# Optimization experiments

Measured on AMD Instinct MI355X. Metric: run time of the kernel, lower is better.

## Reference

```python
import jax, jax.numpy as jnp
import numpy as np

B, R, C, D = 8, 64, 16, 128  # batch, num_rows(taxa), patch_num, embed_dim


def _linear_init(key, fan_in, fan_out):
    lim = 1.0 / np.sqrt(fan_in)
    kw, kb = jax.random.split(key)
    W = jax.random.uniform(kw, (fan_in, fan_out), jnp.float32, -lim, lim)
    b = jax.random.uniform(kb, (fan_out,), jnp.float32, -lim, lim)
    return W, b


def setup_inputs() -> dict:
    key = jax.random.key(0)
    ks = jax.random.split(key, 8)
    row_np, col_np = np.triu_indices(R, k=1)  # n = R*(R-1)/2 = 2016 pairs
    hW, hb = _linear_init(ks[1], D, D)
    gW, gb = _linear_init(ks[2], D, D)
    qW, qb = _linear_init(ks[3], D, D)
    kW, kb = _linear_init(ks[4], D, D)
    s1W, s1b = _linear_init(ks[5], D, D)
    s2W, s2b = _linear_init(ks[6], D, 1)
    return {
        "batch_input": jax.random.normal(ks[0], (B, R, C, D), jnp.float32),
        "seq_mask": jnp.ones((B, 1, C), jnp.float32),
        "row": jnp.asarray(row_np, jnp.int32),
        "col": jnp.asarray(col_np, jnp.int32),
        "hW": hW, "hb": hb, "gW": gW, "gb": gb,
        "qW": qW, "qb": qb, "kW": kW, "kb": kb,
        "s1W": s1W, "s1b": s1b, "s2W": s2W, "s2b": s2b,
    }


def reference(batch_input, seq_mask, row, col,
              hW, hb, gW, gb, qW, qb, kW, kb, s1W, s1b, s2W, s2b):
    b, r, c, d = batch_input.shape
    n = row.shape[0]
    # pairwise gather: x_i, x_j -> [b, n, c, d]
    x_i = batch_input[:, row]
    x_j = batch_input[:, col]
    # sigmoid gate fusion of the pair
    h = (x_i - x_j) @ hW + hb
    z = jax.nn.sigmoid(h)
    x = z * x_i + (1.0 - z) * x_j
    # masked global attention over the batch_input 'memory' (r > 2 branch)
    q = x @ qW + qb                    # [b, n, c, d]
    k = batch_input @ kW + kb          # [b, r, c, d]
    scale = 1.0 / np.sqrt(d * c).astype(np.float32)
    alpha = jnp.einsum('bncd,brcd->bnr', q, k) * scale
    # -inf at (pair n, rows row[n] and col[n]); equivalent to += -inf on finite scores
    neg_mask = (jnp.zeros((n, r), bool)
                .at[jnp.arange(n), row].set(True)
                .at[jnp.arange(n), col].set(True))
    alpha = jnp.where(neg_mask[None], -jnp.inf, alpha)
    alpha = jax.nn.softmax(alpha, axis=-1)
    x_glob = jnp.einsum('bnr,brcd->bncd', alpha, batch_input)
    g = x_glob @ gW + gb
    w = jax.nn.sigmoid(g)
    x = (1.0 - w) * x + w * x_glob
    # s_out: Linear -> GELU(exact) -> Linear(d,1), then mask and reduce over c
    s = jax.nn.gelu(x @ s1W + s1b, approximate=False) @ s2W + s2b  # [b, n, c, 1]
    scores = s[..., 0] * seq_mask       # seq_mask [b,1,c] broadcasts over n
    return scores.sum(-1)               # [b, n]
```

## Files before the change

kernel.cpp:

```cpp
#include <hip/hip_runtime.h>
#include <hip/hip_bf16.h>
#include <math.h>

#define B_    8
#define R_    64
#define C_    16
#define D_    128
#define NPAIR 2016
#define CD    2048
#define PG    16
#define NPG   126
#define XSTR  136
#define LSTR  68
#define NEG_BIG (-1e30f)
#define SCALE 0.022097086912079608f

typedef __attribute__((ext_vector_type(8))) short short8;
typedef __attribute__((ext_vector_type(4))) float float4v;

#define WMH  0u
#define WML  16384u
#define WHH  32768u
#define WHL  49152u
#define WGH  65536u
#define WGL  81920u
#define WSH  98304u
#define VECO 131072u
#define QBKO 131592u
#define MO   132616u
#define XTO  1181192u
#define GTO  2229768u
#define HO   3278344u

__device__ __forceinline__ unsigned short f2b(float f){
    union { float f; unsigned int u; } v; v.f = f;
    const unsigned int r = v.u + 0x7FFFu + ((v.u >> 16) & 1u);
    return (unsigned short)(r >> 16);
}
__device__ __forceinline__ float b2f(unsigned short u){
    union { unsigned int i; float f; } v; v.i = ((unsigned int)u) << 16; return v.f;
}
__device__ __forceinline__ float lo2f(unsigned int u){
    union { unsigned int i; float f; } v; v.i = u << 16; return v.f;
}
__device__ __forceinline__ float hif2f(unsigned int u){
    union { unsigned int i; float f; } v; v.i = u & 0xffff0000u; return v.f;
}
__device__ __forceinline__ unsigned int pack2(float a, float b){
    unsigned int r;
    asm("v_cvt_pk_bf16_f32 %0, %1, %2" : "=v"(r) : "v"(a), "v"(b));
    return r;
}
__device__ __forceinline__ unsigned short f2b1(float a){
    unsigned int r;
    asm("v_cvt_pk_bf16_f32 %0, %1, %1" : "=v"(r) : "v"(a));
    return (unsigned short)r;
}
__device__ __forceinline__ void split_bf(float v, float* hi, float* lo){
    union { float f; unsigned int u; } x; x.f = v;
    const unsigned int r = (x.u + 0x7FFFu + ((x.u >> 16) & 1u)) & 0xffff0000u;
    union { unsigned int u; float f; } h; h.u = r;
    *hi = h.f; *lo = v - h.f;
}
__device__ __forceinline__ float sigmoid_safe(float x){
    return __builtin_amdgcn_rcpf(1.f + __expf(-x));
}
__device__ __forceinline__ float gelu_tanh(float x){
    const float u = x*x;
    const float g2 = x*(1.5957691216057308f + 0.07135481627159f*u);
    return x * sigmoid_safe(g2);
}

__global__ __launch_bounds__(256) void k_prepA(
    const float* __restrict__ x,
    const float* __restrict__ hW, const float* __restrict__ gW,
    const float* __restrict__ qW, const float* __restrict__ qb,
    const float* __restrict__ kW, const float* __restrict__ kb,
    unsigned short* __restrict__ ws)
{
    __shared__ __align__(16) unsigned short tile[128*69];
    const int bid = blockIdx.x, t = threadIdx.x;
    if (bid < 64){
        __shared__ float sKW[2][128];
        const int e0 = bid*2;
        sKW[t>>7][t&127] = kW[(e0 + (t>>7))*128 + (t&127)];
        __syncthreads();
        const int e = t>>7, d = t&127;
        const float* qr = qW + d*128;
        const float* kr = sKW[e];
        float acc = 0.f;
        #pragma unroll 8
        for (int g = 0; g < 128; g += 4){
            const float4 qv = *reinterpret_cast<const float4*>(qr + g);
            acc += qv.x*kr[g] + qv.y*kr[g+1] + qv.z*kr[g+2] + qv.w*kr[g+3];
        }
        float hi, lo; split_bf(acc, &hi, &lo);
        ws[WMH + d*128 + (e0+e)] = f2b(hi);
        ws[WML + d*128 + (e0+e)] = f2b(lo);
    } else if (bid == 64){
        float* vec = (float*)(ws + VECO);
        if (t < 128){
            float a1 = 0.f, a2 = 0.f;
            #pragma unroll 8
            for (int g = 0; g < 128; g += 4){
                const float4 q4 = *reinterpret_cast<const float4*>(qW + t*128 + g);
                const float4 k4 = *reinterpret_cast<const float4*>(kW + t*128 + g);
                const float4 kb4 = *reinterpret_cast<const float4*>(kb + g);
                const float4 qb4 = *reinterpret_cast<const float4*>(qb + g);
                a1 += q4.x*kb4.x + q4.y*kb4.y + q4.z*kb4.z + q4.w*kb4.w;
                a2 += k4.x*qb4.x + k4.y*qb4.y + k4.z*qb4.z + k4.w*qb4.w;
            }
            vec[t] = a1;
            vec[128 + t] = a2;
        } else if (t == 128){
            float a = 0.f;
            for (int g = 0; g < 128; ++g) a = fmaf(qb[g], kb[g], a);
            vec[256] = a;
        }
    } else if (bid < 193){
        const int j = bid - 65;
        const int mat = j >> 6;
        const int gid = (j & 63)*256 + t;
        const int n = gid >> 7, k = gid & 127;
        const float* W = (mat==0) ? hW : gW;
        const unsigned int baseh = (mat==0) ? WHH : WGH;
        const unsigned int basel = (mat==0) ? WHL : WGL;
        float hi, lo; split_bf(W[k*128 + n], &hi, &lo);
        ws[baseh + gid] = f2b(hi);
        ws[basel + gid] = f2b(lo);
    } else {
        const int blk = bid - 193;
        const int b = blk >> 4, cd0 = (blk & 15)*128;
        #pragma unroll
        for (int i = 0; i < 32; ++i){
            const int idx = i*256 + t;
            const int r = idx >> 7, cc = idx & 127;
            tile[cc*69 + r] = f2b(x[((size_t)(b*64 + r))*CD + cd0 + cc]);
        }
        __syncthreads();
        const unsigned int base = XTO + (unsigned int)(b*2048 + cd0)*64;
        #pragma unroll
        for (int j = 0; j < 32; ++j){
            const int idx = j*256 + t;
            const int cc = idx >> 6, r = idx & 63;
            ws[base + cc*64 + r] = tile[cc*69 + r];
        }
    }
}

__global__ __launch_bounds__(512) void k_prepB(const float* __restrict__ x,
        const float* __restrict__ gb, const float* __restrict__ s1W,
        unsigned short* __restrict__ ws)
{
    __shared__ __align__(16) unsigned short smem[8832];
    __shared__ float sQ[4];
    const int bid = blockIdx.x, t = threadIdx.x;
    const int w = t >> 6, lane = t & 63, l15 = lane & 15, quad = lane >> 4;

    if (bid < 256){
        const bool isM = (bid >= 128);
        unsigned short* sH = smem;
        const int br0 = (bid & 127) * 4;
        const float* kqf = (const float*)(ws + VECO) + 128;
        const float* mbf = (const float*)(ws + VECO);
        if (t < 4) sQ[t] = 0.f;
        __syncthreads();
        float qacc[4] = {0.f, 0.f, 0.f, 0.f};
        #pragma unroll
        for (int i = 0; i < 4; ++i){
            const int flat = (t + 512*i)*4;
            const int lr = i;
            const int cd = flat & 2047;
            const float4 v = *reinterpret_cast<const float4*>(x + (size_t)(br0+lr)*CD + cd);
            const int ad = (lr*16 + (cd>>7))*XSTR + lr*8 + (cd & 127);
            uint2 uh;
            uh.x = pack2(v.x, v.y); uh.y = pack2(v.z, v.w);
            *reinterpret_cast<uint2*>(sH + ad) = uh;
            if (isM){
                const float4 kq4 = *reinterpret_cast<const float4*>(kqf + (cd & 127));
                qacc[i] = v.x*kq4.x + v.y*kq4.y + v.z*kq4.z + v.w*kq4.w;
            }
        }
        if (isM){
            #pragma unroll
            for (int i = 0; i < 4; ++i){
                float s = qacc[i];
                #pragma unroll
                for (int off = 1; off < 64; off <<= 1) s += __shfl_xor(s, off);
                if (lane == 0) atomicAdd(&sQ[i], s);
            }
        }
        __syncthreads();
        const unsigned short* Bh = isM ? (ws+WMH) : (ws+WHH);
        const unsigned short* Bl = isM ? (ws+WML) : (ws+WHL);
        const float bv = isM ? mbf[w*16 + l15] : 0.f;
        float4v acc[4];
        #pragma unroll
        for (int mt = 0; mt < 4; ++mt){ float4v d = {bv,bv,bv,bv}; acc[mt] = d; }
        #pragma unroll
        for (int ks = 0; ks < 4; ++ks){
            const int ko = ks*32 + quad*8;
            const int bd = (w*16 + l15)*128 + ko;
            const short8 bh = *reinterpret_cast<const short8*>(Bh + bd);
            const short8 bl = *reinterpret_cast<const short8*>(Bl + bd);
            #pragma unroll
            for (int mt = 0; mt < 4; ++mt){
                const int ad = (mt*16 + l15)*XSTR + mt*8 + ko;
                const short8 ah = *reinterpret_cast<const short8*>(sH + ad);
                float4v d = acc[mt];
                d = __builtin_amdgcn_mfma_f32_16x16x32_bf16(ah, bh, d, 0,0,0);
                d = __builtin_amdgcn_mfma_f32_16x16x32_bf16(ah, bl, d, 0,0,0);
                acc[mt] = d;
            }
        }
        const int f = w*16 + l15;
        const unsigned int dsto = isM ? MO : HO;
        #pragma unroll
        for (int mt = 0; mt < 4; ++mt)
        #pragma unroll
        for (int e = 0; e < 4; ++e){
            const int c = quad*4 + e;
            ws[dsto + (size_t)(br0+mt)*CD + c*128 + f] = f2b(acc[mt][e]);
        }
        if (isM && t < 4){
            const float s0 = ((const float*)(ws + VECO))[256];
            ((float*)(ws + QBKO))[br0 + t] = sQ[t] + 16.f*s0;
        }
    } else if (bid < 384){
        unsigned short* tileB = smem;
        const int gidx = bid - 256;
        const int b = gidx >> 4, cd0 = (gidx & 15)*128;
        #pragma unroll
        for (int i = 0; i < 16; ++i){
            const int idx = i*512 + t;
            const int r = idx >> 7, dd = idx & 127;
            tileB[r*138 + dd] = f2b(x[(size_t)(b*64 + r)*CD + cd0 + dd]);
        }
        __syncthreads();
        float4v acc[4];
        #pragma unroll
        for (int nt = 0; nt < 4; ++nt){ float4v z = {0.f,0.f,0.f,0.f}; acc[nt] = z; }
        #pragma unroll
        for (int ks = 0; ks < 4; ++ks){
            const int ko = ks*32 + quad*8;
            const int adg = (w*16 + l15)*128 + ko;
            const short8 ah = *reinterpret_cast<const short8*>(ws + WGH + adg);
            const short8 al = *reinterpret_cast<const short8*>(ws + WGL + adg);
            #pragma unroll
            for (int nt = 0; nt < 4; ++nt){
                const short8 bb = *reinterpret_cast<const short8*>(tileB + (nt*16 + l15)*138 + ko);
                float4v d = acc[nt];
                d = __builtin_amdgcn_mfma_f32_16x16x32_bf16(ah, bb, d, 0,0,0);
                d = __builtin_amdgcn_mfma_f32_16x16x32_bf16(al, bb, d, 0,0,0);
                acc[nt] = d;
            }
        }
        #pragma unroll
        for (int nt = 0; nt < 4; ++nt)
        #pragma unroll
        for (int e = 0; e < 4; ++e){
            const int f = w*16 + quad*4 + e;
            const float val = acc[nt][e] + gb[f];
            ws[GTO + (size_t)(b*2048 + cd0 + f)*64 + nt*16 + l15] = f2b(val);
        }
    } else {
        const int gid = (bid - 384)*4096 + t;
        #pragma unroll
        for (int i = 0; i < 8; ++i){
            const int g = gid + i*512;
            const int n = g >> 7, k = g & 127;
            ws[WSH + g] = f2b(s1W[k*128 + n]);
        }
    }
}

__global__ __launch_bounds__(512, 4) void k_main(
    const float* __restrict__ x, const float* __restrict__ seq_mask,
    const int* __restrict__ row, const int* __restrict__ col,
    const float* __restrict__ hb, const float* __restrict__ s1b,
    const float* __restrict__ s2W, const float* __restrict__ s2b,
    const unsigned short* __restrict__ ws, float* __restrict__ out)
{
    __shared__ __align__(16) unsigned short sX[256*XSTR + 128];
    __shared__ __align__(16) unsigned short sAl[16*72];
    __shared__ float sLog[16*LSTR];
    __shared__ float sOut[PG];
    __shared__ float sMask[16];
    __shared__ int srp[PG], scp[PG];

    const int t = threadIdx.x;
    const int w = t >> 6, lane = t & 63, l15 = lane & 15, quad = lane >> 4;
    const int b = blockIdx.x, p0 = blockIdx.y * PG;
    const float* xb = x + (size_t)b * R_ * CD;
    const unsigned short* Hb = ws + HO + (size_t)b * R_ * CD;

    if (t < PG){ srp[t] = row[p0+t]; scp[t] = col[p0+t]; sOut[t] = 0.f; }
    if (t >= 32 && t < 48) sMask[t-32] = seq_mask[b*C_ + (t-32)];
    for (int i = t; i < 1152; i += 512) sAl[i] = 0;
    for (int i = t; i < 16*LSTR; i += 512) sLog[i] = 0.f;
    __syncthreads();

    #pragma unroll 4
    for (int i = 0; i < 16; ++i){
        const int flat = (t + 512*i)*4;
        const int p = flat >> 11, cd = flat & 2047;
        const int ri = srp[p], ci = scp[p];
        const float4 xi = *reinterpret_cast<const float4*>(xb + (size_t)ri*CD + cd);
        const float4 xj = *reinterpret_cast<const float4*>(xb + (size_t)ci*CD + cd);
        const uint2 Hi2 = *reinterpret_cast<const uint2*>(Hb + (size_t)ri*CD + cd);
        const uint2 Hj2 = *reinterpret_cast<const uint2*>(Hb + (size_t)ci*CD + cd);
        const float4 h4 = *reinterpret_cast<const float4*>(hb + (cd & 127));
        const float z0 = sigmoid_safe(lo2f(Hi2.x)  - lo2f(Hj2.x)  + h4.x);
        const float z1 = sigmoid_safe(hif2f(Hi2.x) - hif2f(Hj2.x) + h4.y);
        const float z2 = sigmoid_safe(lo2f(Hi2.y)  - lo2f(Hj2.y)  + h4.z);
        const float z3 = sigmoid_safe(hif2f(Hi2.y) - hif2f(Hj2.y) + h4.w);
        const float v0 = xj.x + z0*(xi.x - xj.x);
        const float v1 = xj.y + z1*(xi.y - xj.y);
        const float v2 = xj.z + z2*(xi.z - xj.z);
        const float v3 = xj.w + z3*(xi.w - xj.w);
        const int ad = (p*16 + (cd>>7))*XSTR + p*8 + (cd & 127);
        uint2 uv; uv.x = pack2(v0,v1); uv.y = pack2(v2,v3);
        *reinterpret_cast<uint2*>(sX + ad) = uv;
    }
    __syncthreads();

    {
        const int rt = w & 3, kh = w >> 2;
        const int r = rt*16 + l15;
        const unsigned short* Mr = ws + MO + ((size_t)b*64 + r)*CD + kh*1024;
        float4v d0 = {0.f,0.f,0.f,0.f}, d1 = {0.f,0.f,0.f,0.f};
        float4v d2 = {0.f,0.f,0.f,0.f}, d3 = {0.f,0.f,0.f,0.f};
        #pragma unroll
        for (int ks = 0; ks < 32; ks += 4){
            #pragma unroll
            for (int u = 0; u < 4; ++u){
                const int k = kh*1024 + (ks+u)*32 + quad*8;
                const short8 ah = *reinterpret_cast<const short8*>(
                    sX + (l15*16 + (k>>7))*XSTR + l15*8 + (k & 127));
                const short8 bh = *reinterpret_cast<const short8*>(Mr + (ks+u)*32 + quad*8);
                if (u == 0) d0 = __builtin_amdgcn_mfma_f32_16x16x32_bf16(ah, bh, d0, 0,0,0);
                else if (u == 1) d1 = __builtin_amdgcn_mfma_f32_16x16x32_bf16(ah, bh, d1, 0,0,0);
                else if (u == 2) d2 = __builtin_amdgcn_mfma_f32_16x16x32_bf16(ah, bh, d2, 0,0,0);
                else d3 = __builtin_amdgcn_mfma_f32_16x16x32_bf16(ah, bh, d3, 0,0,0);
            }
        }
        const float4v d = (d0 + d1) + (d2 + d3);
        #pragma unroll
        for (int e = 0; e < 4; ++e){
            const int pp = quad*4 + e;
            atomicAdd(&sLog[pp*LSTR + r], d[e]);
        }
    }
    __syncthreads();

    const unsigned short* XTb = ws + XTO + (size_t)b * CD * 64;
    const unsigned short* GTb = ws + GTO + (size_t)b * CD * 64;
    short8 px0[2], px1[2], pg0[2], pg1[2];
    #pragma unroll
    for (int j = 0; j < 2; ++j){
        const int cd = w*256 + j*16 + l15;
        px0[j] = *reinterpret_cast<const short8*>(XTb + (size_t)cd*64 + quad*8);
        px1[j] = *reinterpret_cast<const short8*>(XTb + (size_t)cd*64 + 32 + quad*8);
        pg0[j] = *reinterpret_cast<const short8*>(GTb + (size_t)cd*64 + quad*8);
        pg1[j] = *reinterpret_cast<const short8*>(GTb + (size_t)cd*64 + 32 + quad*8);
    }

    if (t < 256){
        const int pp = t >> 4, l = t & 15;
        const int ri = srp[pp], ci = scp[pp];
        const float* qbk = (const float*)(ws + QBKO);
        float v[4]; float m = NEG_BIG;
        #pragma unroll
        for (int k = 0; k < 4; ++k){
            const int r = l + 16*k;
            float lv = (sLog[pp*LSTR + r] + qbk[b*64 + r]) * SCALE;
            if (r == ri || r == ci) lv = NEG_BIG;
            v[k] = lv; m = fmaxf(m, lv);
        }
        #pragma unroll
        for (int s = 1; s < 16; s <<= 1) m = fmaxf(m, __shfl_xor(m, s));
        float e4[4]; float sum = 0.f;
        #pragma unroll
        for (int k = 0; k < 4; ++k){
            const int r = l + 16*k;
            const bool masked = (r == ri || r == ci);
            const float e = masked ? 0.f : __expf(fmaxf(v[k]-m, -80.f));
            e4[k] = e; sum += e;
        }
        #pragma unroll
        for (int s = 1; s < 16; s <<= 1) sum += __shfl_xor(sum, s);
        const float inv = __builtin_amdgcn_rcpf(sum);
        #pragma unroll
        for (int k = 0; k < 4; ++k) sAl[pp*72 + l + 16*k] = f2b1(e4[k]*inv);
    }
    __syncthreads();

    {
        const short8 Ah0 = *reinterpret_cast<const short8*>(sAl + l15*72 + quad*8);
        const short8 Ah1 = *reinterpret_cast<const short8*>(sAl + l15*72 + 32 + quad*8);
        #pragma unroll
        for (int j = 0; j < 16; ++j){
            const int s = j & 1;
            float4v dx = {0.f,0.f,0.f,0.f}, dg = {0.f,0.f,0.f,0.f};
            dx = __builtin_amdgcn_mfma_f32_16x16x32_bf16(Ah0, px0[s], dx, 0,0,0);
            dx = __builtin_amdgcn_mfma_f32_16x16x32_bf16(Ah1, px1[s], dx, 0,0,0);
            dg = __builtin_amdgcn_mfma_f32_16x16x32_bf16(Ah0, pg0[s], dg, 0,0,0);
            dg = __builtin_amdgcn_mfma_f32_16x16x32_bf16(Ah1, pg1[s], dg, 0,0,0);
            if (j + 2 < 16){
                const int cd2 = w*256 + (j+2)*16 + l15;
                px0[s] = *reinterpret_cast<const short8*>(XTb + (size_t)cd2*64 + quad*8);
                px1[s] = *reinterpret_cast<const short8*>(XTb + (size_t)cd2*64 + 32 + quad*8);
                pg0[s] = *reinterpret_cast<const short8*>(GTb + (size_t)cd2*64 + quad*8);
                pg1[s] = *reinterpret_cast<const short8*>(GTb + (size_t)cd2*64 + 32 + quad*8);
            }
            const int cd = w*256 + j*16 + l15;
            #pragma unroll
            for (int e = 0; e < 4; ++e){
                const int pp = quad*4 + e;
                const int ad = (pp*16 + (cd>>7))*XSTR + pp*8 + (cd & 127);
                const float wv = sigmoid_safe(dg[e]);
                const float xo = b2f(sX[ad]);
                sX[ad] = f2b1((1.f - wv)*xo + wv*dx[e]);
            }
        }
    }
    __syncthreads();

    {
        float4v acc16[16];
        const float bv = s1b[w*16 + l15];
        #pragma unroll
        for (int mt = 0; mt < 16; ++mt){ float4v d = {bv,bv,bv,bv}; acc16[mt] = d; }
        #pragma unroll
        for (int ks = 0; ks < 4; ++ks){
            const int ko = ks*32 + quad*8;
            const int bd = (w*16 + l15)*128 + ko;
            const short8 bh = *reinterpret_cast<const short8*>(ws + WSH + bd);
            #pragma unroll
            for (int mt = 0; mt < 16; ++mt){
                const short8 a = *reinterpret_cast<const short8*>(sX + (mt*16 + l15)*XSTR + mt*8 + ko);
                acc16[mt] = __builtin_amdgcn_mfma_f32_16x16x32_bf16(a, bh, acc16[mt], 0,0,0);
            }
        }
        const float s2v = s2W[w*16 + l15];
        const float mk0 = sMask[quad*4+0], mk1 = sMask[quad*4+1];
        const float mk2 = sMask[quad*4+2], mk3 = sMask[quad*4+3];
        float psum[16];
        #pragma unroll
        for (int mt = 0; mt < 16; ++mt){
            float s = gelu_tanh(acc16[mt][0]) * mk0;
            s += gelu_tanh(acc16[mt][1]) * mk1;
            s += gelu_tanh(acc16[mt][2]) * mk2;
            s += gelu_tanh(acc16[mt][3]) * mk3;
            psum[mt] = s * s2v;
        }
        #pragma unroll
        for (int s = 1; s < 64; s <<= 1)
            #pragma unroll
            for (int mt = 0; mt < 16; ++mt) psum[mt] += __shfl_xor(psum[mt], s);
        if (lane == 0){
            #pragma unroll
            for (int mt = 0; mt < 16; ++mt) atomicAdd(&sOut[mt], psum[mt]);
        }
    }
    __syncthreads();

    if (t < PG){
        float msum = 0.f;
        #pragma unroll
        for (int c = 0; c < 16; ++c) msum += sMask[c];
        out[(size_t)b*NPAIR + p0 + t] = sOut[t] + s2b[0]*msum;
    }
}

extern "C" void kernel_launch(void* const* d_in, const int* in_sizes, int n_in,
                              void* d_out, int out_size, void* d_ws, size_t ws_size,
                              hipStream_t stream)
{
    const float* x    = (const float*)d_in[0];
    const float* mask = (const float*)d_in[1];
    const int*   row  = (const int*)d_in[2];
    const int*   col  = (const int*)d_in[3];
    const float* hW  = (const float*)d_in[4];  const float* hb  = (const float*)d_in[5];
    const float* gW  = (const float*)d_in[6];  const float* gb  = (const float*)d_in[7];
    const float* qW  = (const float*)d_in[8];  const float* qb  = (const float*)d_in[9];
    const float* kW  = (const float*)d_in[10]; const float* kb  = (const float*)d_in[11];
    const float* s1W = (const float*)d_in[12]; const float* s1b = (const float*)d_in[13];
    const float* s2W = (const float*)d_in[14]; const float* s2b = (const float*)d_in[15];

    unsigned short* ws = (unsigned short*)d_ws;

    k_prepA<<<321, 256, 0, stream>>>(x, hW, gW, qW, qb, kW, kb, ws);
    k_prepB<<<388, 512, 0, stream>>>(x, gb, s1W, ws);
    k_main<<<dim3(B_, NPG), 512, 0, stream>>>(x, mask, row, col,
                                              hb, s1b, s2W, s2b,
                                              ws, (float*)d_out);
}
```

Baseline: 226.1 us.

## Fold hW/gW bf16 splitting and x transpose into prepB; batch B-operand loads

```diff
diff --git a/kernel.cpp b/kernel.cpp
--- a/kernel.cpp
+++ b/kernel.cpp
@@ -20,10 +20,6 @@
 
 #define WMH  0u
 #define WML  16384u
-#define WHH  32768u
-#define WHL  49152u
-#define WGH  65536u
-#define WGL  81920u
 #define WSH  98304u
 #define VECO 131072u
 #define QBKO 131592u
@@ -62,6 +58,13 @@
     union { unsigned int u; float f; } h; h.u = r;
     *hi = h.f; *lo = v - h.f;
 }
+__device__ __forceinline__ void splitw(float v, short* h, short* l){
+    union { float f; unsigned int u; } x; x.f = v;
+    const unsigned int rh = (x.u + 0x7FFFu + ((x.u >> 16) & 1u)) & 0xffff0000u;
+    union { unsigned int u; float f; } hf; hf.u = rh;
+    *h = (short)(rh >> 16);
+    *l = (short)f2b(v - hf.f);
+}
 __device__ __forceinline__ float sigmoid_safe(float x){
     return __builtin_amdgcn_rcpf(1.f + __expf(-x));
 }
@@ -72,13 +75,10 @@
 }
 
 __global__ __launch_bounds__(256) void k_prepA(
-    const float* __restrict__ x,
-    const float* __restrict__ hW, const float* __restrict__ gW,
     const float* __restrict__ qW, const float* __restrict__ qb,
     const float* __restrict__ kW, const float* __restrict__ kb,
     unsigned short* __restrict__ ws)
 {
-    __shared__ __align__(16) unsigned short tile[128*69];
     const int bid = blockIdx.x, t = threadIdx.x;
     if (bid < 64){
         __shared__ float sKW[2][128];
@@ -97,7 +97,7 @@
         float hi, lo; split_bf(acc, &hi, &lo);
         ws[WMH + d*128 + (e0+e)] = f2b(hi);
         ws[WML + d*128 + (e0+e)] = f2b(lo);
-    } else if (bid == 64){
+    } else {
         float* vec = (float*)(ws + VECO);
         if (t < 128){
             float a1 = 0.f, a2 = 0.f;
@@ -117,38 +117,11 @@
             for (int g = 0; g < 128; ++g) a = fmaf(qb[g], kb[g], a);
             vec[256] = a;
         }
-    } else if (bid < 193){
-        const int j = bid - 65;
-        const int mat = j >> 6;
-        const int gid = (j & 63)*256 + t;
-        const int n = gid >> 7, k = gid & 127;
-        const float* W = (mat==0) ? hW : gW;
-        const unsigned int baseh = (mat==0) ? WHH : WGH;
-        const unsigned int basel = (mat==0) ? WHL : WGL;
-        float hi, lo; split_bf(W[k*128 + n], &hi, &lo);
-        ws[baseh + gid] = f2b(hi);
-        ws[basel + gid] = f2b(lo);
-    } else {
-        const int blk = bid - 193;
-        const int b = blk >> 4, cd0 = (blk & 15)*128;
-        #pragma unroll
-        for (int i = 0; i < 32; ++i){
-            const int idx = i*256 + t;
-            const int r = idx >> 7, cc = idx & 127;
-            tile[cc*69 + r] = f2b(x[((size_t)(b*64 + r))*CD + cd0 + cc]);
-        }
-        __syncthreads();
-        const unsigned int base = XTO + (unsigned int)(b*2048 + cd0)*64;
-        #pragma unroll
-        for (int j = 0; j < 32; ++j){
-            const int idx = j*256 + t;
-            const int cc = idx >> 6, r = idx & 63;
-            ws[base + cc*64 + r] = tile[cc*69 + r];
-        }
     }
 }
 
 __global__ __launch_bounds__(512) void k_prepB(const float* __restrict__ x,
+        const float* __restrict__ hW, const float* __restrict__ gW,
         const float* __restrict__ gb, const float* __restrict__ s1W,
         unsigned short* __restrict__ ws)
 {
@@ -191,40 +164,71 @@
             }
         }
         __syncthreads();
-        const unsigned short* Bh = isM ? (ws+WMH) : (ws+WHH);
-        const unsigned short* Bl = isM ? (ws+WML) : (ws+WHL);
-        const float bv = isM ? mbf[w*16 + l15] : 0.f;
-        float4v acc[4];
-        #pragma unroll
-        for (int mt = 0; mt < 4; ++mt){ float4v d = {bv,bv,bv,bv}; acc[mt] = d; }
-        #pragma unroll
-        for (int ks = 0; ks < 4; ++ks){
-            const int ko = ks*32 + quad*8;
-            const int bd = (w*16 + l15)*128 + ko;
-            const short8 bh = *reinterpret_cast<const short8*>(Bh + bd);
-            const short8 bl = *reinterpret_cast<const short8*>(Bl + bd);
-            #pragma unroll
-            for (int mt = 0; mt < 4; ++mt){
-                const int ad = (mt*16 + l15)*XSTR + mt*8 + ko;
-                const short8 ah = *reinterpret_cast<const short8*>(sH + ad);
-                float4v d = acc[mt];
-                d = __builtin_amdgcn_mfma_f32_16x16x32_bf16(ah, bh, d, 0,0,0);
-                d = __builtin_amdgcn_mfma_f32_16x16x32_bf16(ah, bl, d, 0,0,0);
-                acc[mt] = d;
-            }
-        }
-        const int f = w*16 + l15;
-        const unsigned int dsto = isM ? MO : HO;
-        #pragma unroll
-        for (int mt = 0; mt < 4; ++mt)
-        #pragma unroll
-        for (int e = 0; e < 4; ++e){
-            const int c = quad*4 + e;
-            ws[dsto + (size_t)(br0+mt)*CD + c*128 + f] = f2b(acc[mt][e]);
-        }
-        if (isM && t < 4){
-            const float s0 = ((const float*)(ws + VECO))[256];
-            ((float*)(ws + QBKO))[br0 + t] = sQ[t] + 16.f*s0;
+        if (isM){
+            const float bv = mbf[w*16 + l15];
+            float4v acc[4];
+            #pragma unroll
+            for (int mt = 0; mt < 4; ++mt){ float4v d = {bv,bv,bv,bv}; acc[mt] = d; }
+            #pragma unroll
+            for (int ks = 0; ks < 4; ++ks){
+                const int ko = ks*32 + quad*8;
+                const int bd = (w*16 + l15)*128 + ko;
+                const short8 bh = *reinterpret_cast<const short8*>(ws + WMH + bd);
+                const short8 bl = *reinterpret_cast<const short8*>(ws + WML + bd);
+                #pragma unroll
+                for (int mt = 0; mt < 4; ++mt){
+                    const int ad = (mt*16 + l15)*XSTR + mt*8 + ko;
+                    const short8 ah = *reinterpret_cast<const short8*>(sH + ad);
+                    float4v d = acc[mt];
+                    d = __builtin_amdgcn_mfma_f32_16x16x32_bf16(ah, bh, d, 0,0,0);
+                    d = __builtin_amdgcn_mfma_f32_16x16x32_bf16(ah, bl, d, 0,0,0);
+                    acc[mt] = d;
+                }
+            }
+            const int f = w*16 + l15;
+            #pragma unroll
+            for (int mt = 0; mt < 4; ++mt)
+            #pragma unroll
+            for (int e = 0; e < 4; ++e){
+                const int c = quad*4 + e;
+                ws[MO + (size_t)(br0+mt)*CD + c*128 + f] = f2b(acc[mt][e]);
+            }
+            if (t < 4){
+                const float s0 = ((const float*)(ws + VECO))[256];
+                ((float*)(ws + QBKO))[br0 + t] = sQ[t] + 16.f*s0;
+            }
+        } else {
+            const int n = w*16 + l15;
+            float4v acc[4];
+            #pragma unroll
+            for (int mt = 0; mt < 4; ++mt){ float4v z = {0.f,0.f,0.f,0.f}; acc[mt] = z; }
+            #pragma unroll
+            for (int ks = 0; ks < 4; ++ks){
+                const int ko = ks*32 + quad*8;
+                short8 bh, bl;
+                #pragma unroll
+                for (int j = 0; j < 8; ++j){
+                    short hh, ll;
+                    splitw(hW[(size_t)(ko+j)*128 + n], &hh, &ll);
+                    bh[j] = hh; bl[j] = ll;
+                }
+                #pragma unroll
+                for (int mt = 0; mt < 4; ++mt){
+                    const int ad = (mt*16 + l15)*XSTR + mt*8 + ko;
+                    const short8 ah = *reinterpret_cast<const short8*>(sH + ad);
+                    float4v d = acc[mt];
+                    d = __builtin_amdgcn_mfma_f32_16x16x32_bf16(ah, bh, d, 0,0,0);
+                    d = __builtin_amdgcn_mfma_f32_16x16x32_bf16(ah, bl, d, 0,0,0);
+                    acc[mt] = d;
+                }
+            }
+            #pragma unroll
+            for (int mt = 0; mt < 4; ++mt)
+            #pragma unroll
+            for (int e = 0; e < 4; ++e){
+                const int c = quad*4 + e;
+                ws[HO + (size_t)(br0+mt)*CD + c*128 + n] = f2b(acc[mt][e]);
+            }
         }
     } else if (bid < 384){
         unsigned short* tileB = smem;
@@ -237,15 +241,20 @@
             tileB[r*138 + dd] = f2b(x[(size_t)(b*64 + r)*CD + cd0 + dd]);
         }
         __syncthreads();
+        const int fA = w*16 + l15;
         float4v acc[4];
         #pragma unroll
         for (int nt = 0; nt < 4; ++nt){ float4v z = {0.f,0.f,0.f,0.f}; acc[nt] = z; }
         #pragma unroll
         for (int ks = 0; ks < 4; ++ks){
             const int ko = ks*32 + quad*8;
-            const int adg = (w*16 + l15)*128 + ko;
-            const short8 ah = *reinterpret_cast<const short8*>(ws + WGH + adg);
-            const short8 al = *reinterpret_cast<const short8*>(ws + WGL + adg);
+            short8 ah, al;
+            #pragma unroll
+            for (int j = 0; j < 8; ++j){
+                short hh, ll;
+                splitw(gW[(size_t)(ko+j)*128 + fA], &hh, &ll);
+                ah[j] = hh; al[j] = ll;
+            }
             #pragma unroll
             for (int nt = 0; nt < 4; ++nt){
                 const short8 bb = *reinterpret_cast<const short8*>(tileB + (nt*16 + l15)*138 + ko);
@@ -263,13 +272,31 @@
             const float val = acc[nt][e] + gb[f];
             ws[GTO + (size_t)(b*2048 + cd0 + f)*64 + nt*16 + l15] = f2b(val);
         }
-    } else {
+    } else if (bid < 388){
         const int gid = (bid - 384)*4096 + t;
         #pragma unroll
         for (int i = 0; i < 8; ++i){
             const int g = gid + i*512;
             const int n = g >> 7, k = g & 127;
             ws[WSH + g] = f2b(s1W[k*128 + n]);
+        }
+    } else {
+        unsigned short* tile = smem;
+        const int blk = bid - 388;
+        const int b = blk >> 4, cd0 = (blk & 15)*128;
+        #pragma unroll
+        for (int i = 0; i < 16; ++i){
+            const int idx = i*512 + t;
+            const int r = idx >> 7, cc = idx & 127;
+            tile[cc*69 + r] = f2b(x[((size_t)(b*64 + r))*CD + cd0 + cc]);
+        }
+        __syncthreads();
+        const unsigned int base = XTO + (unsigned int)(b*2048 + cd0)*64;
+        #pragma unroll
+        for (int j = 0; j < 16; ++j){
+            const int idx = j*512 + t;
+            const int cc = idx >> 6, r = idx & 63;
+            ws[base + cc*64 + r] = tile[cc*69 + r];
         }
     }
 }
@@ -331,17 +358,20 @@
         float4v d0 = {0.f,0.f,0.f,0.f}, d1 = {0.f,0.f,0.f,0.f};
         float4v d2 = {0.f,0.f,0.f,0.f}, d3 = {0.f,0.f,0.f,0.f};
         #pragma unroll
-        for (int ks = 0; ks < 32; ks += 4){
-            #pragma unroll
-            for (int u = 0; u < 4; ++u){
-                const int k = kh*1024 + (ks+u)*32 + quad*8;
+        for (int h = 0; h < 4; ++h){
+            short8 bhr[8];
+            #pragma unroll
+            for (int u = 0; u < 8; ++u)
+                bhr[u] = *reinterpret_cast<const short8*>(Mr + (h*8+u)*32 + quad*8);
+            #pragma unroll
+            for (int u = 0; u < 8; ++u){
+                const int k = kh*1024 + (h*8+u)*32 + quad*8;
                 const short8 ah = *reinterpret_cast<const short8*>(
                     sX + (l15*16 + (k>>7))*XSTR + l15*8 + (k & 127));
-                const short8 bh = *reinterpret_cast<const short8*>(Mr + (ks+u)*32 + quad*8);
-                if (u == 0) d0 = __builtin_amdgcn_mfma_f32_16x16x32_bf16(ah, bh, d0, 0,0,0);
-                else if (u == 1) d1 = __builtin_amdgcn_mfma_f32_16x16x32_bf16(ah, bh, d1, 0,0,0);
-                else if (u == 2) d2 = __builtin_amdgcn_mfma_f32_16x16x32_bf16(ah, bh, d2, 0,0,0);
-                else d3 = __builtin_amdgcn_mfma_f32_16x16x32_bf16(ah, bh, d3, 0,0,0);
+                if ((u&3) == 0)      d0 = __builtin_amdgcn_mfma_f32_16x16x32_bf16(ah, bhr[u], d0, 0,0,0);
+                else if ((u&3) == 1) d1 = __builtin_amdgcn_mfma_f32_16x16x32_bf16(ah, bhr[u], d1, 0,0,0);
+                else if ((u&3) == 2) d2 = __builtin_amdgcn_mfma_f32_16x16x32_bf16(ah, bhr[u], d2, 0,0,0);
+                else                 d3 = __builtin_amdgcn_mfma_f32_16x16x32_bf16(ah, bhr[u], d3, 0,0,0);
             }
         }
         const float4v d = (d0 + d1) + (d2 + d3);
@@ -431,15 +461,17 @@
         const float bv = s1b[w*16 + l15];
         #pragma unroll
         for (int mt = 0; mt < 16; ++mt){ float4v d = {bv,bv,bv,bv}; acc16[mt] = d; }
+        short8 bh4[4];
+        #pragma unroll
+        for (int ks = 0; ks < 4; ++ks)
+            bh4[ks] = *reinterpret_cast<const short8*>(ws + WSH + (w*16 + l15)*128 + ks*32 + quad*8);
         #pragma unroll
         for (int ks = 0; ks < 4; ++ks){
             const int ko = ks*32 + quad*8;
-            const int bd = (w*16 + l15)*128 + ko;
-            const short8 bh = *reinterpret_cast<const short8*>(ws + WSH + bd);
             #pragma unroll
             for (int mt = 0; mt < 16; ++mt){
                 const short8 a = *reinterpret_cast<const short8*>(sX + (mt*16 + l15)*XSTR + mt*8 + ko);
-                acc16[mt] = __builtin_amdgcn_mfma_f32_16x16x32_bf16(a, bh, acc16[mt], 0,0,0);
+                acc16[mt] = __builtin_amdgcn_mfma_f32_16x16x32_bf16(a, bh4[ks], acc16[mt], 0,0,0);
             }
         }
         const float s2v = s2W[w*16 + l15];
@@ -490,8 +522,8 @@
 
     unsigned short* ws = (unsigned short*)d_ws;
 
-    k_prepA<<<321, 256, 0, stream>>>(x, hW, gW, qW, qb, kW, kb, ws);
-    k_prepB<<<388, 512, 0, stream>>>(x, gb, s1W, ws);
+    k_prepA<<<65, 256, 0, stream>>>(qW, qb, kW, kb, ws);
+    k_prepB<<<516, 512, 0, stream>>>(x, hW, gW, gb, s1W, ws);
     k_main<<<dim3(B_, NPG), 512, 0, stream>>>(x, mask, row, col,
                                               hb, s1b, s2W, s2b,
                                               ws, (float*)d_out);
```

New measurement: 227.3 us. No clear change (+0.5%).
